# Kernel optimization log

Hardware: AMD Instinct MI355X
Metric: run time of the kernel (lower is better)

The kernel has to match this reference:

```python
import jax, jax.numpy as jnp
import numpy as np

DN = ('NCDHW', 'OIDHW', 'NCDHW')

def conv3(x, w):
    # 3x3x3 VALID stencil conv: [1,1,D+2,H+2,W+2] -> [1,1,D,H,W]
    return jax.lax.conv_general_dilated(x, w, (1, 1, 1), 'VALID', dimension_numbers=DN)

def conv_res(x, w):
    # 2x2x2 stride-2 restriction
    return jax.lax.conv_general_dilated(x, w, (2, 2, 2), 'VALID', dimension_numbers=DN)

def prol(x):
    for ax in (2, 3, 4):
        x = jnp.repeat(x, 2, axis=ax)
    return x

def with_halo(x, factor=1.0):
    # apply_BC_* + halo_exchange on one device: edge-replicate a 1-cell halo,
    # optionally scaled by `factor` (apply_BC_u uses -1.0 -> no-slip wall).
    p = jnp.pad(x, ((0, 0), (0, 0), (1, 1), (1, 1), (1, 1)), mode='edge')
    if factor != 1.0:
        interior = jnp.pad(jnp.ones_like(x), ((0, 0), (0, 0), (1, 1), (1, 1), (1, 1)))
        p = p * (interior + factor * (1.0 - interior))
    return p

def pad0(x):
    # apply_BC_cw: zero halo for the multigrid correction
    return jnp.pad(x, ((0, 0), (0, 0), (1, 1), (1, 1), (1, 1)))


def setup_inputs() -> dict:
    key = jax.random.key(0)
    ks = jax.random.split(key, 12)
    D = 128
    shp = (1, 1, D, D, D)
    f32 = jnp.float32
    values_u = jax.random.normal(ks[0], shp, f32)
    values_v = jax.random.normal(ks[1], shp, f32)
    values_w = jax.random.normal(ks[2], shp, f32)
    values_p = jax.random.normal(ks[3], shp, f32)
    sigma = jax.random.uniform(ks[4], shp, f32)
    kshape = (1, 1, 3, 3, 3)
    w_xadv = 0.1 * jax.random.normal(ks[5], kshape, f32)
    w_yadv = 0.1 * jax.random.normal(ks[6], kshape, f32)
    w_zadv = 0.1 * jax.random.normal(ks[7], kshape, f32)
    w_diff = 0.1 * jax.random.normal(ks[8], kshape, f32)
    wA = 0.1 * jax.random.normal(ks[9], kshape, f32)
    wA = wA.at[0, 0, 1, 1, 1].add(-6.0)  # Laplacian-like diagonal so Jacobi division is stable
    w_res = 0.1 * jax.random.normal(ks[10], (1, 1, 2, 2, 2), f32)
    dt = 0.05 * jnp.ones((1,), f32)
    return dict(values_u=values_u, values_v=values_v, values_w=values_w,
                values_p=values_p, sigma=sigma, w_xadv=w_xadv, w_yadv=w_yadv,
                w_zadv=w_zadv, w_diff=w_diff, wA=wA, w_res=w_res, dt=dt,
                iteration=2, nlevel=9)


def reference(values_u, values_v, values_w, values_p, sigma, w_xadv, w_yadv,
              w_zadv, w_diff, wA, w_res, dt, iteration, nlevel):
    diag = wA[0, 0, 1, 1, 1]
    xadv = lambda t: conv3(t, w_xadv)
    yadv = lambda t: conv3(t, w_yadv)
    zadv = lambda t: conv3(t, w_zadv)
    diff = lambda t: conv3(t, w_diff)
    A = lambda t: conv3(t, wA)

    def solid(a, b, c):
        d = 1.0 + dt * sigma
        return a / d, b / d, c / d

    def PG(uu, vv, ww, u, v, w):
        # k_u/k_v/k_w are ones; k_uu/k_vv/k_ww are their BC+halo versions (also ones)
        k_h = with_halo(jnp.ones_like(u))
        k_u = 0.5 * (diff(uu) + diff(uu * k_h) - u * diff(k_h))
        k_v = 0.5 * (diff(vv) + diff(vv * k_h) - v * diff(k_h))
        k_w = 0.5 * (diff(ww) + diff(ww * k_h) - w * diff(k_h))
        return k_u, k_v, k_w

    def f_cycle_mg(uu, vv, wwh, p, pp):
        b = -(xadv(uu) + yadv(vv) + zadv(wwh)) / dt
        w_mg = jnp.zeros((1, 1, 1, 1, 1), p.dtype)
        r = b
        for _ in range(iteration):
            w_mg = jnp.zeros((1, 1, 1, 1, 1), p.dtype)
            r = A(pp) - b
            r_s = [r]
            for _i in range(1, nlevel - 1):
                r = conv_res(r, w_res)
                r_s.append(r)
            for i in reversed(range(1, nlevel - 1)):
                ww_ = pad0(w_mg)
                w_mg = w_mg - A(ww_) / diag + r_s[i] / diag
                w_mg = prol(w_mg)
            p = p - w_mg
            p = p - A(pp) / diag + b / diag
            pp = with_halo(p)
        return p, w_mg, r, pp

    u, v, w = solid(values_u, values_v, values_w)
    uu = with_halo(u, -1.0)
    vv = with_halo(v)
    wwh = with_halo(w)
    pp = with_halo(values_p)

    k_u, k_v, k_w = PG(uu, vv, wwh, u, v, w)
    b_u = u + 0.5 * (0.001 * k_u * dt - u * xadv(uu) * dt - v * yadv(uu) * dt - w * zadv(uu) * dt) - xadv(pp) * dt
    b_v = v + 0.5 * (0.001 * k_v * dt - u * xadv(vv) * dt - v * yadv(vv) * dt - w * zadv(vv) * dt) - yadv(pp) * dt
    b_w = w + 0.5 * (0.001 * k_w * dt - u * xadv(wwh) * dt - v * yadv(wwh) * dt - w * zadv(wwh) * dt) - zadv(pp) * dt
    b_u, b_v, b_w = solid(b_u, b_v, b_w)
    b_uu = with_halo(b_u, -1.0)
    b_vv = with_halo(b_v)
    b_ww = with_halo(b_w)

    k_u, k_v, k_w = PG(b_uu, b_vv, b_ww, b_u, b_v, b_w)
    u = u + 0.001 * k_u * dt - b_u * xadv(b_uu) * dt - b_v * yadv(b_uu) * dt - b_w * zadv(b_uu) * dt - xadv(pp) * dt
    v = v + 0.001 * k_v * dt - b_u * xadv(b_vv) * dt - b_v * yadv(b_vv) * dt - b_w * zadv(b_vv) * dt - yadv(pp) * dt
    w = w + 0.001 * k_w * dt - b_u * xadv(b_ww) * dt - b_v * yadv(b_ww) * dt - b_w * zadv(b_ww) * dt - zadv(pp) * dt
    u, v, w = solid(u, v, w)

    uu = with_halo(u, -1.0)
    vv = with_halo(v)
    wwh = with_halo(w)
    p, w_mg, r, pp = f_cycle_mg(uu, vv, wwh, values_p, pp)

    u = u - xadv(pp) * dt
    v = v - yadv(pp) * dt
    w = w - zadv(pp) * dt
    u, v, w = solid(u, v, w)
    return (u, v, w, p, w_mg, r)
```

## Files before the change

### kernel.cpp

```cpp
#include <hip/hip_runtime.h>


#define NN 128
#define NF (NN*NN*NN)


__device__ __forceinline__ void prep9(int z, int y, int rb[9], bool rn[9]) {
  int zi[3] = {z > 0 ? z-1 : 0, z, z < NN-1 ? z+1 : NN-1};
  int yi[3] = {y > 0 ? y-1 : 0, y, y < NN-1 ? y+1 : NN-1};
  bool zo[3] = {z == 0, false, z == NN-1};
  bool yo[3] = {y == 0, false, y == NN-1};
#pragma unroll
  for (int a = 0; a < 3; ++a)
#pragma unroll
    for (int b = 0; b < 3; ++b) {
      rb[a*3+b] = (zi[a]*NN + yi[b])*NN;
      rn[a*3+b] = zo[a] | yo[b];
    }
}


template<bool NEG>
__device__ __forceinline__ void sten_vel(
    const float* __restrict__ f, const int rb[9], const bool rn[9],
    bool lo, bool hi, int x0,
    const float* __restrict__ w0p, const float* __restrict__ w1p,
    const float* __restrict__ w2p, const float* __restrict__ w3p,
    float acc[4][4], float4* center) {
  const float* const Ws[4] = {w0p, w1p, w2p, w3p};
#pragma unroll
  for (int r = 0; r < 9; ++r) {
    int base = rb[r] + x0;
    float4 c = *(const float4*)(f + base);
    float m1 = f[base - (lo ? 0 : 1)];
    float p4 = f[base + (hi ? 3 : 4)];
    if (NEG) {
      float sr = rn[r] ? -1.f : 1.f;
      m1 *= (rn[r] | lo) ? -1.f : 1.f;
      p4 *= (rn[r] | hi) ? -1.f : 1.f;
      c.x *= sr; c.y *= sr; c.z *= sr; c.w *= sr;
    }
    if (r == 4 && center) *center = c;
    float t[6] = {m1, c.x, c.y, c.z, c.w, p4};
#pragma unroll
    for (int s = 0; s < 4; ++s) {
      const float* W = Ws[s];
      float a0 = W[r*3+0], a1 = W[r*3+1], a2 = W[r*3+2];
#pragma unroll
      for (int k = 0; k < 4; ++k)
        acc[s][k] = fmaf(a0, t[k], fmaf(a1, t[k+1], fmaf(a2, t[k+2], acc[s][k])));
    }
  }
}

__device__ __forceinline__ void sten_p3(
    const float* __restrict__ f, const int rb[9], const bool rn[9],
    bool lo, bool hi, int x0,
    const float* __restrict__ w0p, const float* __restrict__ w1p,
    const float* __restrict__ w2p, float acc[3][4]) {
  const float* const Ws[3] = {w0p, w1p, w2p};
#pragma unroll
  for (int r = 0; r < 9; ++r) {
    int base = rb[r] + x0;
    float4 c = *(const float4*)(f + base);
    float m1 = f[base - (lo ? 0 : 1)];
    float p4 = f[base + (hi ? 3 : 4)];
    float t[6] = {m1, c.x, c.y, c.z, c.w, p4};
#pragma unroll
    for (int s = 0; s < 3; ++s) {
      const float* W = Ws[s];
      float a0 = W[r*3+0], a1 = W[r*3+1], a2 = W[r*3+2];
#pragma unroll
      for (int k = 0; k < 4; ++k)
        acc[s][k] = fmaf(a0, t[k], fmaf(a1, t[k+1], fmaf(a2, t[k+2], acc[s][k])));
    }
  }
}


__global__ void __launch_bounds__(256) k_solid3(
    float* __restrict__ du, float* __restrict__ dv, float* __restrict__ dw,
    const float* __restrict__ su, const float* __restrict__ sv, const float* __restrict__ sw,
    const float* __restrict__ sg, const float* __restrict__ dtp) {
  int i = blockIdx.x*256 + threadIdx.x;
  if (i >= NF/4) return;
  float dt = dtp[0];
  float4 s4 = ((const float4*)sg)[i];
  float4 a4 = ((const float4*)su)[i];
  float4 b4 = ((const float4*)sv)[i];
  float4 c4 = ((const float4*)sw)[i];
  float4 d4 = make_float4(1.f + dt*s4.x, 1.f + dt*s4.y, 1.f + dt*s4.z, 1.f + dt*s4.w);
  ((float4*)du)[i] = make_float4(a4.x/d4.x, a4.y/d4.y, a4.z/d4.z, a4.w/d4.w);
  ((float4*)dv)[i] = make_float4(b4.x/d4.x, b4.y/d4.y, b4.z/d4.z, b4.w/d4.w);
  ((float4*)dw)[i] = make_float4(c4.x/d4.x, c4.y/d4.y, c4.z/d4.z, c4.w/d4.w);
}

__global__ void __launch_bounds__(256) k_mom3(
    float* __restrict__ du, float* __restrict__ dv, float* __restrict__ dw,
    const float* __restrict__ su, const float* __restrict__ sv, const float* __restrict__ sw,
    const float* __restrict__ qu, const float* __restrict__ qv, const float* __restrict__ qw,
    const float* __restrict__ pf, const float* __restrict__ sg,
    const float* __restrict__ wx, const float* __restrict__ wy,
    const float* __restrict__ wz, const float* __restrict__ wd,
    const float* __restrict__ dtp, float scale) {
  int x0 = threadIdx.x * 4;
  int y  = blockIdx.y * 8 + threadIdx.y;
  int z  = blockIdx.x;
  bool lo = (x0 == 0), hi = (x0 == NN-4);
  int rb[9]; bool rn[9];
  prep9(z, y, rb, rn);
  float dt = dtp[0];

  float aU[4][4] = {}, aV[4][4] = {}, aW[4][4] = {}, aP[3][4] = {};
  float4 uc, vc, wc;
  sten_vel<true >(su, rb, rn, lo, hi, x0, wx, wy, wz, wd, aU, &uc);
  sten_vel<false>(sv, rb, rn, lo, hi, x0, wx, wy, wz, wd, aV, &vc);
  sten_vel<false>(sw, rb, rn, lo, hi, x0, wx, wy, wz, wd, aW, &wc);
  sten_p3(pf, rb, rn, lo, hi, x0, wx, wy, wz, aP);

  float sw27 = 0.f;
#pragma unroll
  for (int j = 0; j < 27; ++j) sw27 += wd[j];

  int i4 = ((z*NN + y)*NN + x0) >> 2;
  float4 qu4 = ((const float4*)qu)[i4];
  float4 qv4 = ((const float4*)qv)[i4];
  float4 qw4 = ((const float4*)qw)[i4];
  float4 sg4 = ((const float4*)sg)[i4];
  float ucv[4] = {uc.x, uc.y, uc.z, uc.w};
  float vcv[4] = {vc.x, vc.y, vc.z, vc.w};
  float wcv[4] = {wc.x, wc.y, wc.z, wc.w};
  float qua[4] = {qu4.x, qu4.y, qu4.z, qu4.w};
  float qva[4] = {qv4.x, qv4.y, qv4.z, qv4.w};
  float qwa[4] = {qw4.x, qw4.y, qw4.z, qw4.w};
  float sga[4] = {sg4.x, sg4.y, sg4.z, sg4.w};
  float ou[4], ov[4], ow[4];
#pragma unroll
  for (int k = 0; k < 4; ++k) {
    float ku = aU[3][k] - 0.5f*sw27*ucv[k];
    float kv = aV[3][k] - 0.5f*sw27*vcv[k];
    float kw = aW[3][k] - 0.5f*sw27*wcv[k];
    float ru = qua[k] + scale*dt*(0.001f*ku - ucv[k]*aU[0][k] - vcv[k]*aU[1][k] - wcv[k]*aU[2][k]) - aP[0][k]*dt;
    float rv = qva[k] + scale*dt*(0.001f*kv - ucv[k]*aV[0][k] - vcv[k]*aV[1][k] - wcv[k]*aV[2][k]) - aP[1][k]*dt;
    float rw = qwa[k] + scale*dt*(0.001f*kw - ucv[k]*aW[0][k] - vcv[k]*aW[1][k] - wcv[k]*aW[2][k]) - aP[2][k]*dt;
    float d = 1.0f + dt*sga[k];
    ou[k] = ru/d; ov[k] = rv/d; ow[k] = rw/d;
  }
  ((float4*)du)[i4] = make_float4(ou[0], ou[1], ou[2], ou[3]);
  ((float4*)dv)[i4] = make_float4(ov[0], ov[1], ov[2], ov[3]);
  ((float4*)dw)[i4] = make_float4(ow[0], ow[1], ow[2], ow[3]);
}


__device__ __forceinline__ void row4(const float* __restrict__ f, int base,
                                     bool lo, bool hi, float t[4]) {
  float2 c = *(const float2*)(f + base);
  t[0] = f[base - (lo ? 0 : 1)];
  t[1] = c.x; t[2] = c.y;
  t[3] = f[base + (hi ? 1 : 2)];
}

__device__ __forceinline__ void prep16(int Z, int Y, int rb[16], bool rn[16]) {
  int z0 = 2*Z, y0 = 2*Y;
  int zi[4] = {z0 > 0 ? z0-1 : 0, z0, z0+1, z0+2 < NN ? z0+2 : NN-1};
  int yi[4] = {y0 > 0 ? y0-1 : 0, y0, y0+1, y0+2 < NN ? y0+2 : NN-1};
  bool zo[4] = {Z == 0, false, false, Z == 63};
  bool yo[4] = {Y == 0, false, false, Y == 63};
#pragma unroll
  for (int a = 0; a < 4; ++a)
#pragma unroll
    for (int b = 0; b < 4; ++b) {
      rb[a*4+b] = (zi[a]*NN + yi[b])*NN;
      rn[a*4+b] = zo[a] | yo[b];
    }
}

template<bool NEG>
__device__ __forceinline__ void load16(const float* __restrict__ f,
    const int rb[16], const bool rn[16], bool lo, bool hi, int x0, float t[16][4]) {
#pragma unroll
  for (int r = 0; r < 16; ++r) {
    row4(f, rb[r] + x0, lo, hi, t[r]);
    if (NEG) {
      float sr = rn[r] ? -1.f : 1.f;
      t[r][0] *= (rn[r] | lo) ? -1.f : 1.f;
      t[r][3] *= (rn[r] | hi) ? -1.f : 1.f;
      t[r][1] *= sr; t[r][2] *= sr;
    }
  }
}

__device__ __forceinline__ void dots8(const float t[16][4],
                                      const float* __restrict__ W, float s8[8]) {
#pragma unroll
  for (int dz = 0; dz < 2; ++dz)
#pragma unroll
    for (int dy = 0; dy < 2; ++dy)
#pragma unroll
      for (int dx = 0; dx < 2; ++dx) {
        float s = 0.f;
#pragma unroll
        for (int a = 0; a < 3; ++a)
#pragma unroll
          for (int b = 0; b < 3; ++b)
#pragma unroll
            for (int c = 0; c < 3; ++c)
              s = fmaf(W[(a*3+b)*3+c], t[(dz+a)*4 + dy+b][dx+c], s);
        s8[(dz*2+dy)*2+dx] += s;
      }
}

__global__ void __launch_bounds__(256) k_bdiv_resres(
    float* __restrict__ bb, float* __restrict__ rfine, float* __restrict__ rc1,
    const float* __restrict__ su, const float* __restrict__ sv, const float* __restrict__ sw,
    const float* __restrict__ pf,
    const float* __restrict__ wx, const float* __restrict__ wy, const float* __restrict__ wz,
    const float* __restrict__ wA, const float* __restrict__ wr,
    const float* __restrict__ dtp) {
  int i = blockIdx.x*256 + threadIdx.x;
  if (i >= 64*64*64) return;
  int X = i & 63, Y = (i >> 6) & 63, Z = i >> 12;
  bool lo = (X == 0), hi = (X == 63);
  int x0 = 2*X;
  int rb[16]; bool rn[16];
  prep16(Z, Y, rb, rn);
  float rdt = 1.0f / dtp[0];

  float s8[8] = {};
  {
    float t[16][4];
    load16<true >(su, rb, rn, lo, hi, x0, t); dots8(t, wx, s8);
  }
  {
    float t[16][4];
    load16<false>(sv, rb, rn, lo, hi, x0, t); dots8(t, wy, s8);
  }
  {
    float t[16][4];
    load16<false>(sw, rb, rn, lo, hi, x0, t); dots8(t, wz, s8);
  }
  float a8[8] = {};
  {
    float t[16][4];
    load16<false>(pf, rb, rn, lo, hi, x0, t); dots8(t, wA, a8);
  }
  float rsum = 0.f;
#pragma unroll
  for (int f = 0; f < 8; ++f) {
    int dz = f >> 2, dy = (f >> 1) & 1, dx = f & 1;
    float bcell = -s8[f] * rdt;
    float rcell = a8[f] - bcell;
    int idx = ((2*Z+dz)*NN + (2*Y+dy))*NN + x0 + dx;
    bb[idx] = bcell;
    rfine[idx] = rcell;
    rsum = fmaf(wr[(dz*2+dy)*2+dx], rcell, rsum);
  }
  rc1[i] = rsum;
}

__global__ void __launch_bounds__(256) k_resres1(
    float* __restrict__ rfine, float* __restrict__ rc1,
    const float* __restrict__ pf, const float* __restrict__ bb,
    const float* __restrict__ wA, const float* __restrict__ wr) {
  int i = blockIdx.x*256 + threadIdx.x;
  if (i >= 64*64*64) return;
  int X = i & 63, Y = (i >> 6) & 63, Z = i >> 12;
  bool lo = (X == 0), hi = (X == 63);
  int x0 = 2*X;
  int rb[16]; bool rn[16];
  prep16(Z, Y, rb, rn);
  float a8[8] = {};
  {
    float t[16][4];
    load16<false>(pf, rb, rn, lo, hi, x0, t); dots8(t, wA, a8);
  }
  float rsum = 0.f;
#pragma unroll
  for (int f = 0; f < 8; ++f) {
    int dz = f >> 2, dy = (f >> 1) & 1, dx = f & 1;
    int idx = ((2*Z+dz)*NN + (2*Y+dy))*NN + x0 + dx;
    float rcell = a8[f] - bb[idx];
    rfine[idx] = rcell;
    rsum = fmaf(wr[(dz*2+dy)*2+dx], rcell, rsum);
  }
  rc1[i] = rsum;
}

__global__ void __launch_bounds__(256) k_restrict(
    float* __restrict__ dst, const float* __restrict__ src,
    const float* __restrict__ wr, int no) {
  int i = blockIdx.x*256 + threadIdx.x;
  int n3 = no*no*no;
  if (i >= n3) return;
  int x = i % no; int t = i / no; int y = t % no; int z = t / no;
  int ni = 2*no;
  float s = 0.f;
#pragma unroll
  for (int a = 0; a < 2; ++a)
#pragma unroll
    for (int b = 0; b < 2; ++b)
#pragma unroll
      for (int c = 0; c < 2; ++c)
        s = fmaf(wr[(a*2+b)*2+c], src[((2*z+a)*ni + (2*y+b))*ni + (2*x+c)], s);
  dst[i] = s;
}

__device__ __forceinline__ float azb_prol(const float* __restrict__ wh, int hs, int s,
    int z, int y, int x, const float* __restrict__ wA) {
  float acc = 0.f;
#pragma unroll
  for (int a = 0; a < 3; ++a) { int zz = z + a - 1; if ((unsigned)zz >= (unsigned)s) continue;
#pragma unroll
    for (int b = 0; b < 3; ++b) { int yy = y + b - 1; if ((unsigned)yy >= (unsigned)s) continue;
#pragma unroll
      for (int c = 0; c < 3; ++c) { int xx = x + c - 1; if ((unsigned)xx >= (unsigned)s) continue;
        acc = fmaf(wA[(a*3+b)*3+c], wh[((zz>>1)*hs + (yy>>1))*hs + (xx>>1)], acc);
      } } }
  return acc;
}

__global__ void __launch_bounds__(512) k_mg_small(
    float* __restrict__ w16, float* __restrict__ r_o,
    const float* __restrict__ rc2,
    const float* __restrict__ wA, const float* __restrict__ wr) {
  __shared__ float r16[4096];
  __shared__ float r8[512];
  __shared__ float r4[64];
  __shared__ float r2[8];
  __shared__ float wa[512];
  __shared__ float wb[64];
  __shared__ float scal[2];
  int tid = threadIdx.x;
  float diag = wA[13];
  float wrl[8];
#pragma unroll
  for (int j = 0; j < 8; ++j) wrl[j] = wr[j];

  for (int j = tid; j < 4096; j += 512) {
    int x = j & 15, y = (j >> 4) & 15, z = j >> 8;
    float s = 0.f;
#pragma unroll
    for (int a = 0; a < 2; ++a)
#pragma unroll
      for (int b = 0; b < 2; ++b)
#pragma unroll
        for (int c = 0; c < 2; ++c)
          s = fmaf(wrl[(a*2+b)*2+c], rc2[((2*z+a)*32 + (2*y+b))*32 + (2*x+c)], s);
    r16[j] = s;
  }
  __syncthreads();
  {
    int j = tid;
    int x = j & 7, y = (j >> 3) & 7, z = j >> 6;
    float s = 0.f;
#pragma unroll
    for (int a = 0; a < 2; ++a)
#pragma unroll
      for (int b = 0; b < 2; ++b)
#pragma unroll
        for (int c = 0; c < 2; ++c)
          s = fmaf(wrl[(a*2+b)*2+c], r16[((2*z+a)*16 + (2*y+b))*16 + (2*x+c)], s);
    r8[j] = s;
  }
  __syncthreads();
  if (tid < 64) {
    int x = tid & 3, y = (tid >> 2) & 3, z = tid >> 4;
    float s = 0.f;
#pragma unroll
    for (int a = 0; a < 2; ++a)
#pragma unroll
      for (int b = 0; b < 2; ++b)
#pragma unroll
        for (int c = 0; c < 2; ++c)
          s = fmaf(wrl[(a*2+b)*2+c], r8[((2*z+a)*8 + (2*y+b))*8 + (2*x+c)], s);
    r4[tid] = s;
  }
  __syncthreads();
  if (tid < 8) {
    int x = tid & 1, y = (tid >> 1) & 1, z = tid >> 2;
    float s = 0.f;
#pragma unroll
    for (int a = 0; a < 2; ++a)
#pragma unroll
      for (int b = 0; b < 2; ++b)
#pragma unroll
        for (int c = 0; c < 2; ++c)
          s = fmaf(wrl[(a*2+b)*2+c], r4[((2*z+a)*4 + (2*y+b))*4 + (2*x+c)], s);
    r2[tid] = s;
  }
  __syncthreads();
  if (tid == 0) {
    float s = 0.f;
#pragma unroll
    for (int j = 0; j < 8; ++j) s = fmaf(wrl[j], r2[j], s);
    scal[0] = s;
    r_o[0] = s;
    scal[1] = s / diag;
  }
  __syncthreads();
  if (tid < 8) {
    int x = tid & 1, y = (tid >> 1) & 1, z = tid >> 2;
    float wp = scal[1];
    float az = azb_prol(&scal[1], 1, 2, z, y, x, wA);
    wa[tid] = wp - az/diag + r2[tid]/diag;
  }
  __syncthreads();
  if (tid < 64) {
    int x = tid & 3, y = (tid >> 2) & 3, z = tid >> 4;
    float wp = wa[((z>>1)*2 + (y>>1))*2 + (x>>1)];
    float az = azb_prol(wa, 2, 4, z, y, x, wA);
    wb[tid] = wp - az/diag + r4[tid]/diag;
  }
  __syncthreads();
  {
    int j = tid;
    int x = j & 7, y = (j >> 3) & 7, z = j >> 6;
    float wp = wb[((z>>1)*4 + (y>>1))*4 + (x>>1)];
    float az = azb_prol(wb, 4, 8, z, y, x, wA);
    wa[j] = wp - az/diag + r8[j]/diag;
  }
  __syncthreads();
  for (int j = tid; j < 4096; j += 512) {
    int x = j & 15, y = (j >> 4) & 15, z = j >> 8;
    float wp = wa[((z>>1)*8 + (y>>1))*8 + (x>>1)];
    float az = azb_prol(wa, 8, 16, z, y, x, wA);
    w16[j] = wp - az/diag + r16[j]/diag;
  }
}

__global__ void __launch_bounds__(256) k_coarse_step(
    float* __restrict__ wout, const float* __restrict__ wh,
    const float* __restrict__ rl, const float* __restrict__ wA, int s) {
  int i = blockIdx.x*256 + threadIdx.x;
  int n3 = s*s*s;
  if (i >= n3) return;
  int x = i % s; int t = i / s; int y = t % s; int z = t / s;
  int hs = s >> 1;
  float diag = wA[13];
  float wp = wh[((z>>1)*hs + (y>>1))*hs + (x>>1)];
  float az = azb_prol(wh, hs, s, z, y, x, wA);
  wout[i] = wp - az/diag + rl[i]/diag;
}

__global__ void __launch_bounds__(256) k_pupd4(
    float* __restrict__ pdst, float* __restrict__ wmgo,
    const float* __restrict__ psrc, const float* __restrict__ rfine,
    const float* __restrict__ w64, const float* __restrict__ wA, int writeWmg) {
  int i4 = blockIdx.x*256 + threadIdx.x;
  if (i4 >= NF/4) return;
  int i = i4*4;
  int x = i & (NN-1); int t = i >> 7; int y = t & (NN-1); int z = t >> 7;
  float rdiag = 1.0f / wA[13];
  float2 w2 = *(const float2*)(w64 + ((size_t)(z>>1)*64 + (y>>1))*64 + (x>>1));
  float4 ps = ((const float4*)psrc)[i4];
  float4 rf = ((const float4*)rfine)[i4];
  float4 o = make_float4(ps.x - w2.x - rf.x*rdiag,
                         ps.y - w2.x - rf.y*rdiag,
                         ps.z - w2.y - rf.z*rdiag,
                         ps.w - w2.y - rf.w*rdiag);
  ((float4*)pdst)[i4] = o;
  if (writeWmg) ((float4*)wmgo)[i4] = make_float4(w2.x, w2.x, w2.y, w2.y);
}

__global__ void __launch_bounds__(256) k_proj3(
    float* __restrict__ u, float* __restrict__ v, float* __restrict__ w,
    const float* __restrict__ pf, const float* __restrict__ sg,
    const float* __restrict__ wx, const float* __restrict__ wy,
    const float* __restrict__ wz, const float* __restrict__ dtp) {
  int x0 = threadIdx.x * 4;
  int y  = blockIdx.y * 8 + threadIdx.y;
  int z  = blockIdx.x;
  bool lo = (x0 == 0), hi = (x0 == NN-4);
  int rb[9]; bool rn[9];
  prep9(z, y, rb, rn);
  float aP[3][4] = {};
  sten_p3(pf, rb, rn, lo, hi, x0, wx, wy, wz, aP);
  float dt = dtp[0];
  int i4 = ((z*NN + y)*NN + x0) >> 2;
  float4 u4 = ((const float4*)u)[i4];
  float4 v4 = ((const float4*)v)[i4];
  float4 w4 = ((const float4*)w)[i4];
  float4 sg4 = ((const float4*)sg)[i4];
  float ua[4] = {u4.x, u4.y, u4.z, u4.w};
  float va[4] = {v4.x, v4.y, v4.z, v4.w};
  float wa[4] = {w4.x, w4.y, w4.z, w4.w};
  float sa[4] = {sg4.x, sg4.y, sg4.z, sg4.w};
  float ou[4], ov[4], ow[4];
#pragma unroll
  for (int k = 0; k < 4; ++k) {
    float d = 1.0f + dt*sa[k];
    ou[k] = (ua[k] - aP[0][k]*dt)/d;
    ov[k] = (va[k] - aP[1][k]*dt)/d;
    ow[k] = (wa[k] - aP[2][k]*dt)/d;
  }
  ((float4*)u)[i4] = make_float4(ou[0], ou[1], ou[2], ou[3]);
  ((float4*)v)[i4] = make_float4(ov[0], ov[1], ov[2], ov[3]);
  ((float4*)w)[i4] = make_float4(ow[0], ow[1], ow[2], ow[3]);
}


extern "C" void kernel_launch(void* const* d_in, const int* in_sizes, int n_in,
                              void* d_out, int out_size, void* d_ws, size_t ws_size,
                              hipStream_t stream) {
  const float* values_u = (const float*)d_in[0];
  const float* values_v = (const float*)d_in[1];
  const float* values_w = (const float*)d_in[2];
  const float* values_p = (const float*)d_in[3];
  const float* sigma    = (const float*)d_in[4];
  const float* wx       = (const float*)d_in[5];
  const float* wy       = (const float*)d_in[6];
  const float* wz       = (const float*)d_in[7];
  const float* wd       = (const float*)d_in[8];
  const float* wA       = (const float*)d_in[9];
  const float* wr       = (const float*)d_in[10];
  const float* dtp      = (const float*)d_in[11];

  float* out   = (float*)d_out;
  float* u_o   = out;
  float* v_o   = out + (size_t)NF;
  float* w_o   = out + (size_t)2*NF;
  float* p_o   = out + (size_t)3*NF;
  float* wmg_o = out + (size_t)4*NF;
  float* r_o   = out + (size_t)5*NF;

  float* ws    = (float*)d_ws;
  float* f0    = ws;
  float* f1    = f0 + (size_t)NF;
  float* f2    = f1 + (size_t)NF;
  float* bws   = f2 + (size_t)NF;
  float* rfine = bws + (size_t)NF;
  float* pbuf  = rfine + (size_t)NF;
  float* rc1   = pbuf + (size_t)NF;
  float* rc2   = rc1 + 262144;
  float* w16   = rc2 + 32768;
  float* w32   = w16 + 4096;
  float* w64   = w32 + 32768;

  const int TB = 256;
  dim3 blkS(32, 8, 1);
  dim3 grdS(128, 16, 1);

  k_solid3<<<NF/4/TB, TB, 0, stream>>>(u_o, v_o, w_o, values_u, values_v, values_w, sigma, dtp);
  k_mom3<<<grdS, blkS, 0, stream>>>(f0, f1, f2, u_o, v_o, w_o, u_o, v_o, w_o,
                                    values_p, sigma, wx, wy, wz, wd, dtp, 0.5f);
  k_mom3<<<grdS, blkS, 0, stream>>>(u_o, v_o, w_o, f0, f1, f2, u_o, v_o, w_o,
                                    values_p, sigma, wx, wy, wz, wd, dtp, 1.0f);

  k_bdiv_resres<<<1024, TB, 0, stream>>>(bws, rfine, rc1, u_o, v_o, w_o, values_p,
                                         wx, wy, wz, wA, wr, dtp);
  k_restrict<<<128, TB, 0, stream>>>(rc2, rc1, wr, 32);
  k_mg_small<<<1, 512, 0, stream>>>(w16, r_o, rc2, wA, wr);
  k_coarse_step<<<128, TB, 0, stream>>>(w32, w16, rc2, wA, 32);
  k_coarse_step<<<1024, TB, 0, stream>>>(w64, w32, rc1, wA, 64);
  k_pupd4<<<NF/4/TB, TB, 0, stream>>>(pbuf, wmg_o, values_p, rfine, w64, wA, 0);

  k_resres1<<<1024, TB, 0, stream>>>(rfine, rc1, pbuf, bws, wA, wr);
  k_restrict<<<128, TB, 0, stream>>>(rc2, rc1, wr, 32);
  k_mg_small<<<1, 512, 0, stream>>>(w16, r_o, rc2, wA, wr);
  k_coarse_step<<<128, TB, 0, stream>>>(w32, w16, rc2, wA, 32);
  k_coarse_step<<<1024, TB, 0, stream>>>(w64, w32, rc1, wA, 64);
  k_pupd4<<<NF/4/TB, TB, 0, stream>>>(p_o, wmg_o, pbuf, rfine, w64, wA, 1);

  k_proj3<<<grdS, blkS, 0, stream>>>(u_o, v_o, w_o, p_o, sigma, wx, wy, wz, dtp);
}
```

Measured before the change: 242.6 us.

## Widen fine-grid residual/restriction tiles and reorder stencil loads into z-phases

The fused divergence/residual/restriction kernels now give each thread an 8-wide by 2x2 (z,y) block of fine cells. Rows are loaded as float4 pairs and reused across the two z and two y outputs, and stores are vectorized; the grid shrinks from 1024 to 256 blocks. The momentum stencils load three rows at a time before accumulating, the first momentum pass reuses the centre values instead of reloading q, and divisions become reciprocal-multiplies. The aim is fewer redundant global loads and narrower memory ops, at the cost of more registers per thread and far fewer threads in the residual kernels.

Result: slower. 259.5 us (+7.0%).

```diff
diff --git a/kernel.cpp b/kernel.cpp
--- a/kernel.cpp
+++ b/kernel.cpp
@@ -19,61 +19,40 @@
     }
 }
 
-
-template<bool NEG>
-__device__ __forceinline__ void sten_vel(
+template<bool NEG, int NSET>
+__device__ __forceinline__ void sten_phased(
     const float* __restrict__ f, const int rb[9], const bool rn[9],
-    bool lo, bool hi, int x0,
-    const float* __restrict__ w0p, const float* __restrict__ w1p,
-    const float* __restrict__ w2p, const float* __restrict__ w3p,
-    float acc[4][4], float4* center) {
-  const float* const Ws[4] = {w0p, w1p, w2p, w3p};
-#pragma unroll
-  for (int r = 0; r < 9; ++r) {
-    int base = rb[r] + x0;
-    float4 c = *(const float4*)(f + base);
-    float m1 = f[base - (lo ? 0 : 1)];
-    float p4 = f[base + (hi ? 3 : 4)];
-    if (NEG) {
-      float sr = rn[r] ? -1.f : 1.f;
-      m1 *= (rn[r] | lo) ? -1.f : 1.f;
-      p4 *= (rn[r] | hi) ? -1.f : 1.f;
-      c.x *= sr; c.y *= sr; c.z *= sr; c.w *= sr;
+    bool lo, bool hi, int x0, const float* const Ws[NSET],
+    float acc[][4], float4* center) {
+#pragma unroll
+  for (int a = 0; a < 3; ++a) {
+    float t[3][6];
+#pragma unroll
+    for (int b = 0; b < 3; ++b) {
+      int r = a*3 + b;
+      int base = rb[r] + x0;
+      float4 c = *(const float4*)(f + base);
+      float m1 = f[base - (lo ? 0 : 1)];
+      float p4 = f[base + (hi ? 3 : 4)];
+      if (NEG) {
+        float sr = rn[r] ? -1.f : 1.f;
+        m1 *= (rn[r] | lo) ? -1.f : 1.f;
+        p4 *= (rn[r] | hi) ? -1.f : 1.f;
+        c.x *= sr; c.y *= sr; c.z *= sr; c.w *= sr;
+      }
+      t[b][0]=m1; t[b][1]=c.x; t[b][2]=c.y; t[b][3]=c.z; t[b][4]=c.w; t[b][5]=p4;
     }
-    if (r == 4 && center) *center = c;
-    float t[6] = {m1, c.x, c.y, c.z, c.w, p4};
-#pragma unroll
-    for (int s = 0; s < 4; ++s) {
-      const float* W = Ws[s];
-      float a0 = W[r*3+0], a1 = W[r*3+1], a2 = W[r*3+2];
-#pragma unroll
-      for (int k = 0; k < 4; ++k)
-        acc[s][k] = fmaf(a0, t[k], fmaf(a1, t[k+1], fmaf(a2, t[k+2], acc[s][k])));
-    }
-  }
-}
-
-__device__ __forceinline__ void sten_p3(
-    const float* __restrict__ f, const int rb[9], const bool rn[9],
-    bool lo, bool hi, int x0,
-    const float* __restrict__ w0p, const float* __restrict__ w1p,
-    const float* __restrict__ w2p, float acc[3][4]) {
-  const float* const Ws[3] = {w0p, w1p, w2p};
-#pragma unroll
-  for (int r = 0; r < 9; ++r) {
-    int base = rb[r] + x0;
-    float4 c = *(const float4*)(f + base);
-    float m1 = f[base - (lo ? 0 : 1)];
-    float p4 = f[base + (hi ? 3 : 4)];
-    float t[6] = {m1, c.x, c.y, c.z, c.w, p4};
-#pragma unroll
-    for (int s = 0; s < 3; ++s) {
-      const float* W = Ws[s];
-      float a0 = W[r*3+0], a1 = W[r*3+1], a2 = W[r*3+2];
-#pragma unroll
-      for (int k = 0; k < 4; ++k)
-        acc[s][k] = fmaf(a0, t[k], fmaf(a1, t[k+1], fmaf(a2, t[k+2], acc[s][k])));
-    }
+    if (a == 1 && center) *center = make_float4(t[1][1], t[1][2], t[1][3], t[1][4]);
+#pragma unroll
+    for (int b = 0; b < 3; ++b)
+#pragma unroll
+      for (int s = 0; s < NSET; ++s) {
+        const float* W = Ws[s];
+        float a0 = W[(a*3+b)*3+0], a1 = W[(a*3+b)*3+1], a2 = W[(a*3+b)*3+2];
+#pragma unroll
+        for (int k = 0; k < 4; ++k)
+          acc[s][k] = fmaf(a0, t[b][k], fmaf(a1, t[b][k+1], fmaf(a2, t[b][k+2], acc[s][k])));
+      }
   }
 }
 
@@ -89,12 +68,14 @@
   float4 a4 = ((const float4*)su)[i];
   float4 b4 = ((const float4*)sv)[i];
   float4 c4 = ((const float4*)sw)[i];
-  float4 d4 = make_float4(1.f + dt*s4.x, 1.f + dt*s4.y, 1.f + dt*s4.z, 1.f + dt*s4.w);
-  ((float4*)du)[i] = make_float4(a4.x/d4.x, a4.y/d4.y, a4.z/d4.z, a4.w/d4.w);
-  ((float4*)dv)[i] = make_float4(b4.x/d4.x, b4.y/d4.y, b4.z/d4.z, b4.w/d4.w);
-  ((float4*)dw)[i] = make_float4(c4.x/d4.x, c4.y/d4.y, c4.z/d4.z, c4.w/d4.w);
-}
-
+  float4 r4 = make_float4(1.f/(1.f + dt*s4.x), 1.f/(1.f + dt*s4.y),
+                          1.f/(1.f + dt*s4.z), 1.f/(1.f + dt*s4.w));
+  ((float4*)du)[i] = make_float4(a4.x*r4.x, a4.y*r4.y, a4.z*r4.z, a4.w*r4.w);
+  ((float4*)dv)[i] = make_float4(b4.x*r4.x, b4.y*r4.y, b4.z*r4.z, b4.w*r4.w);
+  ((float4*)dw)[i] = make_float4(c4.x*r4.x, c4.y*r4.y, c4.z*r4.z, c4.w*r4.w);
+}
+
+template<bool QALIAS>
 __global__ void __launch_bounds__(256) k_mom3(
     float* __restrict__ du, float* __restrict__ dv, float* __restrict__ dw,
     const float* __restrict__ su, const float* __restrict__ sv, const float* __restrict__ sw,
@@ -110,29 +91,37 @@
   int rb[9]; bool rn[9];
   prep9(z, y, rb, rn);
   float dt = dtp[0];
+  const float* Wv[4] = {wx, wy, wz, wd};
+  const float* Wp[3] = {wx, wy, wz};
 
   float aU[4][4] = {}, aV[4][4] = {}, aW[4][4] = {}, aP[3][4] = {};
   float4 uc, vc, wc;
-  sten_vel<true >(su, rb, rn, lo, hi, x0, wx, wy, wz, wd, aU, &uc);
-  sten_vel<false>(sv, rb, rn, lo, hi, x0, wx, wy, wz, wd, aV, &vc);
-  sten_vel<false>(sw, rb, rn, lo, hi, x0, wx, wy, wz, wd, aW, &wc);
-  sten_p3(pf, rb, rn, lo, hi, x0, wx, wy, wz, aP);
+  sten_phased<true , 4>(su, rb, rn, lo, hi, x0, Wv, aU, &uc);
+  sten_phased<false, 4>(sv, rb, rn, lo, hi, x0, Wv, aV, &vc);
+  sten_phased<false, 4>(sw, rb, rn, lo, hi, x0, Wv, aW, &wc);
+  sten_phased<false, 3>(pf, rb, rn, lo, hi, x0, Wp, aP, (float4*)nullptr);
 
   float sw27 = 0.f;
 #pragma unroll
   for (int j = 0; j < 27; ++j) sw27 += wd[j];
 
   int i4 = ((z*NN + y)*NN + x0) >> 2;
-  float4 qu4 = ((const float4*)qu)[i4];
-  float4 qv4 = ((const float4*)qv)[i4];
-  float4 qw4 = ((const float4*)qw)[i4];
   float4 sg4 = ((const float4*)sg)[i4];
   float ucv[4] = {uc.x, uc.y, uc.z, uc.w};
   float vcv[4] = {vc.x, vc.y, vc.z, vc.w};
   float wcv[4] = {wc.x, wc.y, wc.z, wc.w};
-  float qua[4] = {qu4.x, qu4.y, qu4.z, qu4.w};
-  float qva[4] = {qv4.x, qv4.y, qv4.z, qv4.w};
-  float qwa[4] = {qw4.x, qw4.y, qw4.z, qw4.w};
+  float qua[4], qva[4], qwa[4];
+  if (QALIAS) {
+#pragma unroll
+    for (int k = 0; k < 4; ++k) { qua[k]=ucv[k]; qva[k]=vcv[k]; qwa[k]=wcv[k]; }
+  } else {
+    float4 qu4 = ((const float4*)qu)[i4];
+    float4 qv4 = ((const float4*)qv)[i4];
+    float4 qw4 = ((const float4*)qw)[i4];
+    qua[0]=qu4.x; qua[1]=qu4.y; qua[2]=qu4.z; qua[3]=qu4.w;
+    qva[0]=qv4.x; qva[1]=qv4.y; qva[2]=qv4.z; qva[3]=qv4.w;
+    qwa[0]=qw4.x; qwa[1]=qw4.y; qwa[2]=qw4.z; qwa[3]=qw4.w;
+  }
   float sga[4] = {sg4.x, sg4.y, sg4.z, sg4.w};
   float ou[4], ov[4], ow[4];
 #pragma unroll
@@ -143,8 +132,8 @@
     float ru = qua[k] + scale*dt*(0.001f*ku - ucv[k]*aU[0][k] - vcv[k]*aU[1][k] - wcv[k]*aU[2][k]) - aP[0][k]*dt;
     float rv = qva[k] + scale*dt*(0.001f*kv - ucv[k]*aV[0][k] - vcv[k]*aV[1][k] - wcv[k]*aV[2][k]) - aP[1][k]*dt;
     float rw = qwa[k] + scale*dt*(0.001f*kw - ucv[k]*aW[0][k] - vcv[k]*aW[1][k] - wcv[k]*aW[2][k]) - aP[2][k]*dt;
-    float d = 1.0f + dt*sga[k];
-    ou[k] = ru/d; ov[k] = rv/d; ow[k] = rw/d;
+    float rd = 1.0f / (1.0f + dt*sga[k]);
+    ou[k] = ru*rd; ov[k] = rv*rd; ow[k] = rw*rd;
   }
   ((float4*)du)[i4] = make_float4(ou[0], ou[1], ou[2], ou[3]);
   ((float4*)dv)[i4] = make_float4(ov[0], ov[1], ov[2], ov[3]);
@@ -152,65 +141,64 @@
 }
 
 
-__device__ __forceinline__ void row4(const float* __restrict__ f, int base,
-                                     bool lo, bool hi, float t[4]) {
-  float2 c = *(const float2*)(f + base);
-  t[0] = f[base - (lo ? 0 : 1)];
-  t[1] = c.x; t[2] = c.y;
-  t[3] = f[base + (hi ? 1 : 2)];
-}
-
-__device__ __forceinline__ void prep16(int Z, int Y, int rb[16], bool rn[16]) {
-  int z0 = 2*Z, y0 = 2*Y;
-  int zi[4] = {z0 > 0 ? z0-1 : 0, z0, z0+1, z0+2 < NN ? z0+2 : NN-1};
-  int yi[4] = {y0 > 0 ? y0-1 : 0, y0, y0+1, y0+2 < NN ? y0+2 : NN-1};
-  bool zo[4] = {Z == 0, false, false, Z == 63};
-  bool yo[4] = {Y == 0, false, false, Y == 63};
+template<bool NEG>
+__device__ __forceinline__ void cc_field(
+    const float* __restrict__ f, const float* __restrict__ W,
+    const int rb16[16], const bool zn[4], const bool yn[4],
+    bool lo, bool hi, int fx0, float acc[2][2][8]) {
+#pragma unroll
+  for (int zp = 0; zp < 4; ++zp) {
+    float t[4][10];
+#pragma unroll
+    for (int yp = 0; yp < 4; ++yp) {
+      int base = rb16[zp*4+yp] + fx0;
+      float4 A = *(const float4*)(f + base);
+      float4 B = *(const float4*)(f + base + 4);
+      float m1 = f[base - (lo ? 0 : 1)];
+      float p8 = f[base + (hi ? 7 : 8)];
+      float* tr = t[yp];
+      tr[0]=m1; tr[1]=A.x; tr[2]=A.y; tr[3]=A.z; tr[4]=A.w;
+      tr[5]=B.x; tr[6]=B.y; tr[7]=B.z; tr[8]=B.w; tr[9]=p8;
+      if (NEG) {
+        bool rno = zn[zp] | yn[yp];
+        float sr = rno ? -1.f : 1.f;
+#pragma unroll
+        for (int q = 1; q <= 8; ++q) tr[q] *= sr;
+        tr[0] *= (rno | lo) ? -1.f : 1.f;
+        tr[9] *= (rno | hi) ? -1.f : 1.f;
+      }
+    }
+#pragma unroll
+    for (int dz = 0; dz < 2; ++dz) {
+      int a = zp - dz;
+      if (a < 0 || a > 2) continue;
+#pragma unroll
+      for (int oy = 0; oy < 2; ++oy)
+#pragma unroll
+        for (int b = 0; b < 3; ++b) {
+          const float* tr = t[oy + b];
+          float w0 = W[(a*3+b)*3+0], w1 = W[(a*3+b)*3+1], w2 = W[(a*3+b)*3+2];
+#pragma unroll
+          for (int k = 0; k < 8; ++k)
+            acc[dz][oy][k] = fmaf(w0, tr[k], fmaf(w1, tr[k+1], fmaf(w2, tr[k+2], acc[dz][oy][k])));
+        }
+    }
+  }
+}
+
+__device__ __forceinline__ void cc_prep(int Z, int Y, int rb16[16], bool zn[4], bool yn[4]) {
+  int fz[4] = {2*Z > 0 ? 2*Z-1 : 0, 2*Z, 2*Z+1, 2*Z+2 < NN ? 2*Z+2 : NN-1};
+  int fy[4] = {2*Y > 0 ? 2*Y-1 : 0, 2*Y, 2*Y+1, 2*Y+2 < NN ? 2*Y+2 : NN-1};
+  zn[0] = (Z == 0); zn[1] = zn[2] = false; zn[3] = (Z == 63);
+  yn[0] = (Y == 0); yn[1] = yn[2] = false; yn[3] = (Y == 63);
 #pragma unroll
   for (int a = 0; a < 4; ++a)
 #pragma unroll
-    for (int b = 0; b < 4; ++b) {
-      rb[a*4+b] = (zi[a]*NN + yi[b])*NN;
-      rn[a*4+b] = zo[a] | yo[b];
-    }
-}
-
-template<bool NEG>
-__device__ __forceinline__ void load16(const float* __restrict__ f,
-    const int rb[16], const bool rn[16], bool lo, bool hi, int x0, float t[16][4]) {
-#pragma unroll
-  for (int r = 0; r < 16; ++r) {
-    row4(f, rb[r] + x0, lo, hi, t[r]);
-    if (NEG) {
-      float sr = rn[r] ? -1.f : 1.f;
-      t[r][0] *= (rn[r] | lo) ? -1.f : 1.f;
-      t[r][3] *= (rn[r] | hi) ? -1.f : 1.f;
-      t[r][1] *= sr; t[r][2] *= sr;
-    }
-  }
-}
-
-__device__ __forceinline__ void dots8(const float t[16][4],
-                                      const float* __restrict__ W, float s8[8]) {
-#pragma unroll
-  for (int dz = 0; dz < 2; ++dz)
-#pragma unroll
-    for (int dy = 0; dy < 2; ++dy)
-#pragma unroll
-      for (int dx = 0; dx < 2; ++dx) {
-        float s = 0.f;
-#pragma unroll
-        for (int a = 0; a < 3; ++a)
-#pragma unroll
-          for (int b = 0; b < 3; ++b)
-#pragma unroll
-            for (int c = 0; c < 3; ++c)
-              s = fmaf(W[(a*3+b)*3+c], t[(dz+a)*4 + dy+b][dx+c], s);
-        s8[(dz*2+dy)*2+dx] += s;
-      }
-}
-
-__global__ void __launch_bounds__(256) k_bdiv_resres(
+    for (int b = 0; b < 4; ++b)
+      rb16[a*4+b] = (fz[a]*NN + fy[b])*NN;
+}
+
+__global__ void __launch_bounds__(256) k_bdivres(
     float* __restrict__ bb, float* __restrict__ rfine, float* __restrict__ rc1,
     const float* __restrict__ su, const float* __restrict__ sv, const float* __restrict__ sw,
     const float* __restrict__ pf,
@@ -218,44 +206,42 @@
     const float* __restrict__ wA, const float* __restrict__ wr,
     const float* __restrict__ dtp) {
   int i = blockIdx.x*256 + threadIdx.x;
-  if (i >= 64*64*64) return;
-  int X = i & 63, Y = (i >> 6) & 63, Z = i >> 12;
-  bool lo = (X == 0), hi = (X == 63);
-  int x0 = 2*X;
-  int rb[16]; bool rn[16];
-  prep16(Z, Y, rb, rn);
+  int Xq = i & 15, Y = (i >> 4) & 63, Z = i >> 10;
+  int fx0 = Xq*8;
+  bool lo = (Xq == 0), hi = (Xq == 15);
+  int rb16[16]; bool zn[4], yn[4];
+  cc_prep(Z, Y, rb16, zn, yn);
+
+  float bs[2][2][8] = {}, ap[2][2][8] = {};
+  cc_field<true >(su, wx, rb16, zn, yn, lo, hi, fx0, bs);
+  cc_field<false>(sv, wy, rb16, zn, yn, lo, hi, fx0, bs);
+  cc_field<false>(sw, wz, rb16, zn, yn, lo, hi, fx0, bs);
+  cc_field<false>(pf, wA, rb16, zn, yn, lo, hi, fx0, ap);
+
   float rdt = 1.0f / dtp[0];
-
-  float s8[8] = {};
-  {
-    float t[16][4];
-    load16<true >(su, rb, rn, lo, hi, x0, t); dots8(t, wx, s8);
-  }
-  {
-    float t[16][4];
-    load16<false>(sv, rb, rn, lo, hi, x0, t); dots8(t, wy, s8);
-  }
-  {
-    float t[16][4];
-    load16<false>(sw, rb, rn, lo, hi, x0, t); dots8(t, wz, s8);
-  }
-  float a8[8] = {};
-  {
-    float t[16][4];
-    load16<false>(pf, rb, rn, lo, hi, x0, t); dots8(t, wA, a8);
-  }
-  float rsum = 0.f;
-#pragma unroll
-  for (int f = 0; f < 8; ++f) {
-    int dz = f >> 2, dy = (f >> 1) & 1, dx = f & 1;
-    float bcell = -s8[f] * rdt;
-    float rcell = a8[f] - bcell;
-    int idx = ((2*Z+dz)*NN + (2*Y+dy))*NN + x0 + dx;
-    bb[idx] = bcell;
-    rfine[idx] = rcell;
-    rsum = fmaf(wr[(dz*2+dy)*2+dx], rcell, rsum);
-  }
-  rc1[i] = rsum;
+  float rs[4] = {};
+#pragma unroll
+  for (int dz = 0; dz < 2; ++dz)
+#pragma unroll
+    for (int oy = 0; oy < 2; ++oy) {
+      int fi = ((2*Z+dz)*NN + 2*Y+oy)*NN + fx0;
+      float bv[8], rv[8];
+#pragma unroll
+      for (int k = 0; k < 8; ++k) {
+        bv[k] = -bs[dz][oy][k]*rdt;
+        rv[k] = ap[dz][oy][k] - bv[k];
+      }
+      *(float4*)(bb+fi)      = make_float4(bv[0],bv[1],bv[2],bv[3]);
+      *(float4*)(bb+fi+4)    = make_float4(bv[4],bv[5],bv[6],bv[7]);
+      *(float4*)(rfine+fi)   = make_float4(rv[0],rv[1],rv[2],rv[3]);
+      *(float4*)(rfine+fi+4) = make_float4(rv[4],rv[5],rv[6],rv[7]);
+#pragma unroll
+      for (int cq = 0; cq < 4; ++cq)
+#pragma unroll
+        for (int dx = 0; dx < 2; ++dx)
+          rs[cq] = fmaf(wr[(dz*2+oy)*2+dx], rv[2*cq+dx], rs[cq]);
+    }
+  *(float4*)(rc1 + ((size_t)(Z*64+Y)*64 + Xq*4)) = make_float4(rs[0],rs[1],rs[2],rs[3]);
 }
 
 __global__ void __launch_bounds__(256) k_resres1(
@@ -263,27 +249,36 @@
     const float* __restrict__ pf, const float* __restrict__ bb,
     const float* __restrict__ wA, const float* __restrict__ wr) {
   int i = blockIdx.x*256 + threadIdx.x;
-  if (i >= 64*64*64) return;
-  int X = i & 63, Y = (i >> 6) & 63, Z = i >> 12;
-  bool lo = (X == 0), hi = (X == 63);
-  int x0 = 2*X;
-  int rb[16]; bool rn[16];
-  prep16(Z, Y, rb, rn);
-  float a8[8] = {};
-  {
-    float t[16][4];
-    load16<false>(pf, rb, rn, lo, hi, x0, t); dots8(t, wA, a8);
-  }
-  float rsum = 0.f;
-#pragma unroll
-  for (int f = 0; f < 8; ++f) {
-    int dz = f >> 2, dy = (f >> 1) & 1, dx = f & 1;
-    int idx = ((2*Z+dz)*NN + (2*Y+dy))*NN + x0 + dx;
-    float rcell = a8[f] - bb[idx];
-    rfine[idx] = rcell;
-    rsum = fmaf(wr[(dz*2+dy)*2+dx], rcell, rsum);
-  }
-  rc1[i] = rsum;
+  int Xq = i & 15, Y = (i >> 4) & 63, Z = i >> 10;
+  int fx0 = Xq*8;
+  bool lo = (Xq == 0), hi = (Xq == 15);
+  int rb16[16]; bool zn[4], yn[4];
+  cc_prep(Z, Y, rb16, zn, yn);
+
+  float ap[2][2][8] = {};
+  cc_field<false>(pf, wA, rb16, zn, yn, lo, hi, fx0, ap);
+
+  float rs[4] = {};
+#pragma unroll
+  for (int dz = 0; dz < 2; ++dz)
+#pragma unroll
+    for (int oy = 0; oy < 2; ++oy) {
+      int fi = ((2*Z+dz)*NN + 2*Y+oy)*NN + fx0;
+      float4 b0 = *(const float4*)(bb+fi);
+      float4 b1 = *(const float4*)(bb+fi+4);
+      float bv[8] = {b0.x,b0.y,b0.z,b0.w,b1.x,b1.y,b1.z,b1.w};
+      float rv[8];
+#pragma unroll
+      for (int k = 0; k < 8; ++k) rv[k] = ap[dz][oy][k] - bv[k];
+      *(float4*)(rfine+fi)   = make_float4(rv[0],rv[1],rv[2],rv[3]);
+      *(float4*)(rfine+fi+4) = make_float4(rv[4],rv[5],rv[6],rv[7]);
+#pragma unroll
+      for (int cq = 0; cq < 4; ++cq)
+#pragma unroll
+        for (int dx = 0; dx < 2; ++dx)
+          rs[cq] = fmaf(wr[(dz*2+oy)*2+dx], rv[2*cq+dx], rs[cq]);
+    }
+  *(float4*)(rc1 + ((size_t)(Z*64+Y)*64 + Xq*4)) = make_float4(rs[0],rs[1],rs[2],rs[3]);
 }
 
 __global__ void __launch_bounds__(256) k_restrict(
@@ -473,8 +468,9 @@
   bool lo = (x0 == 0), hi = (x0 == NN-4);
   int rb[9]; bool rn[9];
   prep9(z, y, rb, rn);
+  const float* Wp[3] = {wx, wy, wz};
   float aP[3][4] = {};
-  sten_p3(pf, rb, rn, lo, hi, x0, wx, wy, wz, aP);
+  sten_phased<false, 3>(pf, rb, rn, lo, hi, x0, Wp, aP, (float4*)nullptr);
   float dt = dtp[0];
   int i4 = ((z*NN + y)*NN + x0) >> 2;
   float4 u4 = ((const float4*)u)[i4];
@@ -488,10 +484,10 @@
   float ou[4], ov[4], ow[4];
 #pragma unroll
   for (int k = 0; k < 4; ++k) {
-    float d = 1.0f + dt*sa[k];
-    ou[k] = (ua[k] - aP[0][k]*dt)/d;
-    ov[k] = (va[k] - aP[1][k]*dt)/d;
-    ow[k] = (wa[k] - aP[2][k]*dt)/d;
+    float rd = 1.0f / (1.0f + dt*sa[k]);
+    ou[k] = (ua[k] - aP[0][k]*dt)*rd;
+    ov[k] = (va[k] - aP[1][k]*dt)*rd;
+    ow[k] = (wa[k] - aP[2][k]*dt)*rd;
   }
   ((float4*)u)[i4] = make_float4(ou[0], ou[1], ou[2], ou[3]);
   ((float4*)v)[i4] = make_float4(ov[0], ov[1], ov[2], ov[3]);
@@ -541,20 +537,20 @@
   dim3 grdS(128, 16, 1);
 
   k_solid3<<<NF/4/TB, TB, 0, stream>>>(u_o, v_o, w_o, values_u, values_v, values_w, sigma, dtp);
-  k_mom3<<<grdS, blkS, 0, stream>>>(f0, f1, f2, u_o, v_o, w_o, u_o, v_o, w_o,
-                                    values_p, sigma, wx, wy, wz, wd, dtp, 0.5f);
-  k_mom3<<<grdS, blkS, 0, stream>>>(u_o, v_o, w_o, f0, f1, f2, u_o, v_o, w_o,
-                                    values_p, sigma, wx, wy, wz, wd, dtp, 1.0f);
-
-  k_bdiv_resres<<<1024, TB, 0, stream>>>(bws, rfine, rc1, u_o, v_o, w_o, values_p,
-                                         wx, wy, wz, wA, wr, dtp);
+  k_mom3<true ><<<grdS, blkS, 0, stream>>>(f0, f1, f2, u_o, v_o, w_o, u_o, v_o, w_o,
+                                           values_p, sigma, wx, wy, wz, wd, dtp, 0.5f);
+  k_mom3<false><<<grdS, blkS, 0, stream>>>(u_o, v_o, w_o, f0, f1, f2, u_o, v_o, w_o,
+                                           values_p, sigma, wx, wy, wz, wd, dtp, 1.0f);
+
+  k_bdivres<<<256, TB, 0, stream>>>(bws, rfine, rc1, u_o, v_o, w_o, values_p,
+                                    wx, wy, wz, wA, wr, dtp);
   k_restrict<<<128, TB, 0, stream>>>(rc2, rc1, wr, 32);
   k_mg_small<<<1, 512, 0, stream>>>(w16, r_o, rc2, wA, wr);
   k_coarse_step<<<128, TB, 0, stream>>>(w32, w16, rc2, wA, 32);
   k_coarse_step<<<1024, TB, 0, stream>>>(w64, w32, rc1, wA, 64);
   k_pupd4<<<NF/4/TB, TB, 0, stream>>>(pbuf, wmg_o, values_p, rfine, w64, wA, 0);
 
-  k_resres1<<<1024, TB, 0, stream>>>(rfine, rc1, pbuf, bws, wA, wr);
+  k_resres1<<<256, TB, 0, stream>>>(rfine, rc1, pbuf, bws, wA, wr);
   k_restrict<<<128, TB, 0, stream>>>(rc2, rc1, wr, 32);
   k_mg_small<<<1, 512, 0, stream>>>(w16, r_o, rc2, wA, wr);
   k_coarse_step<<<128, TB, 0, stream>>>(w32, w16, rc2, wA, 32);
```
